# Optimization experiments

Hardware: AMD Instinct MI355X
Metric: run time of the kernel (lower is better)

The kernel has to match this reference:

```python
import jax, jax.numpy as jnp
import numpy as np

B_GRAPHS = 32   # number of graphs in the batch (static)
HEADS = 8
EPS = 1e-8


def _layer_norm(x, g, b):
    mu = x.mean(-1, keepdims=True)
    var = x.var(-1, keepdims=True)
    return (x - mu) * jax.lax.rsqrt(var + 1e-5) * g + b


def setup_inputs() -> dict:
    key = jax.random.key(0)
    ks = jax.random.split(key, 16)
    N, C, d, M = 5120, 128, 16, 256
    E = N * 16
    f32 = jnp.float32
    sc_c = 1.0 / np.sqrt(C)
    inp = {
        'x': jax.random.normal(ks[0], (N, C), f32),
        'pe_re': jax.random.normal(ks[1], (N, d), f32),
        'pe_im': jax.random.normal(ks[2], (N, d), f32),
        'wq': jax.random.normal(ks[3], (C, C), f32) * sc_c,
        'bq': jnp.zeros((C,), f32),
        'wk': jax.random.normal(ks[4], (C, C), f32) * sc_c,
        'bk': jnp.zeros((C,), f32),
        'wv': jax.random.normal(ks[5], (C, C), f32) * sc_c,
        'bv': jnp.zeros((C,), f32),
        'wo': jax.random.normal(ks[6], (C, C), f32) * sc_c,
        'bo': jnp.zeros((C,), f32),
        'pe_w1': jax.random.normal(ks[7], (4 * d, 2 * d), f32) * (1.0 / np.sqrt(4 * d)),
        'pe_b1': jnp.zeros((2 * d,), f32),
        'pe_w2': jax.random.normal(ks[8], (2 * d, HEADS), f32) * (1.0 / np.sqrt(2 * d)),
        'pe_b2': jnp.zeros((HEADS,), f32),
        'mlp_w1': jax.random.normal(ks[9], (C, 2 * C), f32) * sc_c,
        'mlp_b1': jnp.zeros((2 * C,), f32),
        'mlp_w2': jax.random.normal(ks[10], (2 * C, C), f32) * (1.0 / np.sqrt(2 * C)),
        'mlp_b2': jnp.zeros((C,), f32),
        'ln2_g': jnp.ones((C,), f32),
        'ln2_b': jnp.zeros((C,), f32),
        'ln3_g': jnp.ones((C,), f32),
        'ln3_b': jnp.zeros((C,), f32),
        'batch': jnp.sort(jax.random.randint(ks[11], (N,), 0, B_GRAPHS, jnp.int32)),
        'edge_index': jax.random.randint(ks[12], (2, E), 0, N, jnp.int32),
        'nmax': M,
    }
    return inp


def reference(x, pe_re, pe_im, wq, bq, wk, bk, wv, bv, wo, bo,
              pe_w1, pe_b1, pe_w2, pe_b2, mlp_w1, mlp_b1, mlp_w2, mlp_b2,
              ln2_g, ln2_b, ln3_g, ln3_b, batch, edge_index, nmax):
    N, C = x.shape
    H = HEADS
    dh = C // H
    M = nmax

    # --- to_dense_batch: ragged [N,*] -> dense [B, M, *] + mask ---
    counts = jax.ops.segment_sum(jnp.ones((N,), jnp.int32), batch, num_segments=B_GRAPHS)
    offsets = jnp.concatenate([jnp.zeros((1,), jnp.int32), jnp.cumsum(counts)[:-1]])
    intra = jnp.arange(N, dtype=jnp.int32) - offsets[batch]
    hd = jnp.zeros((B_GRAPHS, M, C), x.dtype).at[batch, intra].set(x)
    ar = jnp.zeros((B_GRAPHS, M, pe_re.shape[1]), x.dtype).at[batch, intra].set(pe_re)
    ai = jnp.zeros((B_GRAPHS, M, pe_im.shape[1]), x.dtype).at[batch, intra].set(pe_im)
    mask = jnp.zeros((B_GRAPHS, M), bool).at[batch, intra].set(True)

    # --- pairwise complex-angle PE bias ---
    pn = jnp.sqrt(ar * ar + ai * ai + EPS)                 # [B,M,d] complex_norm
    denom = pn[:, :, None, :] * pn[:, None, :, :] + EPS    # [B,M,M,d]
    # z_i * conj(z_j) normalized -> cos/sin of pairwise angle
    real = (ar[:, :, None, :] * ar[:, None, :, :] + ai[:, :, None, :] * ai[:, None, :, :]) / denom
    imag = (ai[:, :, None, :] * ar[:, None, :, :] - ar[:, :, None, :] * ai[:, None, :, :]) / denom
    pni = jnp.broadcast_to(pn[:, :, None, :], real.shape)
    pnj = jnp.broadcast_to(pn[:, None, :, :], real.shape)
    bias_in = jnp.concatenate([pni, pnj, real, imag], axis=-1)       # [B,M,M,4d]
    hb = jax.nn.relu(bias_in @ pe_w1 + pe_b1) @ pe_w2 + pe_b2        # [B,M,M,H]
    # torch: bias.transpose(1,-1) swaps dims 1 and 3 -> [B,H,M,M]
    bias = jnp.transpose(hb, (0, 3, 2, 1))                           # [B,H,q,k]

    # --- multi-head attention with float bias + key padding mask ---
    q = (hd @ wq + bq).reshape(B_GRAPHS, M, H, dh)
    k = (hd @ wk + bk).reshape(B_GRAPHS, M, H, dh)
    v = (hd @ wv + bv).reshape(B_GRAPHS, M, H, dh)
    scores = jnp.einsum('bihd,bjhd->bhij', q, k) / np.sqrt(dh) + bias
    scores = jnp.where(mask[:, None, None, :], scores, -1e9)
    attn = jax.nn.softmax(scores, axis=-1)
    o = jnp.einsum('bhij,bjhd->bihd', attn, v).reshape(B_GRAPHS, M, C)
    o = o @ wo + bo

    # --- back to ragged, residual, norms, FFN ---
    h = o[batch, intra] + x
    h = _layer_norm(h, ln2_g, ln2_b)
    out = h + (jax.nn.relu(h @ mlp_w1 + mlp_b1) @ mlp_w2 + mlp_b2)
    out = _layer_norm(out, ln3_g, ln3_b)
    return out
```

## Files before the change

### kernel.cpp

```cpp
#include <hip/hip_runtime.h>

#define N_NODES 5120
#define C_DIM   128
#define D_PE    16
#define M_MAX   256
#define B_G     32
#define H_HEADS 8
#define DH      16
#define EPS_PE  1e-8f
#define QT      2
#define SCP     264

#define WS_COUNTS   0
#define WS_OFFSETS  32
#define WS_INTRA    64
#define WS_MASK     5184
#define WS_CN       13376
#define WS_PN       275520
#define WS_KFHI     406592
#define WS_KFLO     668736
#define WS_QM       799808
#define WS_KM       1848384
#define WS_VM       2896960
#define WS_OATT     3945536
#define WS_HLN      4994112
#define WS_FFNH     5649472
#define WS_BIAS     6960192
#define WS_WPK_HI   15348800
#define WS_WPK_LO   15414336
#define WS_ZERO_FLOATS 13376

#define WOFF_O   49152
#define WOFF_W1  65536
#define WOFF_W2  98304

typedef __attribute__((ext_vector_type(8))) short bf8_t;
typedef __attribute__((ext_vector_type(4))) float f4_t;

__device__ inline short f2bf(float f) {
    union { float f; unsigned u; } v; v.f = f;
    unsigned r = (v.u + 0x7FFF + ((v.u >> 16) & 1)) >> 16;
    return (short)r;
}
__device__ inline float bf2f(short h) {
    union { unsigned u; float f; } v; v.u = ((unsigned)(unsigned short)h) << 16;
    return v.f;
}
__device__ inline unsigned pack2(short a, short b) {
    return (unsigned)(unsigned short)a | ((unsigned)(unsigned short)b << 16);
}
__device__ inline bf8_t bf8_from2(uint2 a, uint2 b) {
    bf8_t o;
    o[0]=(short)a.x; o[1]=(short)(a.x>>16); o[2]=(short)a.y; o[3]=(short)(a.y>>16);
    o[4]=(short)b.x; o[5]=(short)(b.x>>16); o[6]=(short)b.y; o[7]=(short)(b.y>>16);
    return o;
}

__global__ __launch_bounds__(256) void setup_kernel(
    const int* __restrict__ batch, int* __restrict__ counts_o,
    int* __restrict__ offsets, int* __restrict__ intra)
{
    __shared__ int cnt[B_G];
    __shared__ int off[B_G];
    const int t = threadIdx.x;
    if (t < B_G) cnt[t] = 0;
    __syncthreads();
    for (int n = t; n < N_NODES; n += 256) atomicAdd(&cnt[batch[n]], 1);
    __syncthreads();
    if (t == 0) { int s = 0; for (int b = 0; b < B_G; ++b) { off[b] = s; s += cnt[b]; } }
    __syncthreads();
    if (t < B_G) { offsets[t] = off[t]; counts_o[t] = cnt[t]; }
    for (int n = t; n < N_NODES; n += 256) intra[n] = n - off[batch[n]];
}

__global__ __launch_bounds__(256) void prep_kernel(
    const float* __restrict__ pre, const float* __restrict__ pim,
    const int* __restrict__ batch, const int* __restrict__ intra,
    float* __restrict__ pn, float* __restrict__ cn,
    unsigned short* __restrict__ kf_hi, unsigned short* __restrict__ kf_lo,
    int* __restrict__ mask)
{
    const int idx = blockIdx.x * 256 + threadIdx.x;
    const int n = idx >> 4, dd = idx & 15;
    const int b = batch[n], m = intra[n];
    const size_t cell = (size_t)b * M_MAX + m;
    const float a = pre[(size_t)n * D_PE + dd], bb = pim[(size_t)n * D_PE + dd];
    const float p = sqrtf(a * a + bb * bb + EPS_PE);
    const float inv = 1.f / p;
    const float cr = a * inv, ci = bb * inv;
    pn[cell * 16 + dd] = p;
    cn[cell * 32 + dd]      = cr;
    cn[cell * 32 + 16 + dd] = ci;
    const size_t hb = cell * 64, lb = cell * 32;
    short crh = f2bf(cr), cih = f2bf(ci);
    kf_hi[hb + dd]      = (unsigned short)crh;
    kf_hi[hb + 16 + dd] = (unsigned short)cih;
    kf_hi[hb + 32 + dd] = (unsigned short)f2bf(p);
    kf_hi[hb + 48 + dd] = (dd == 0) ? (unsigned short)f2bf(1.f) : 0;
    kf_lo[lb + dd]      = (unsigned short)f2bf(cr - bf2f(crh));
    kf_lo[lb + 16 + dd] = (unsigned short)f2bf(ci - bf2f(cih));
    if (dd == 0) mask[cell] = 1;
}

__global__ __launch_bounds__(256) void wpack_kernel(
    const float* __restrict__ wq, const float* __restrict__ wk,
    const float* __restrict__ wv, const float* __restrict__ wo,
    const float* __restrict__ w1, const float* __restrict__ w2,
    unsigned short* __restrict__ hi, unsigned short* __restrict__ lo)
{
    const int tid = blockIdx.x * 256 + threadIdx.x;
    const int tile = tid >> 6, lane = tid & 63;
    const float* W; int N, ltile; size_t off;
    if (tile < 128) {
        const int wi = tile >> 5; ltile = tile & 31; N = 128;
        W = (wi == 0) ? wq : (wi == 1) ? wk : (wi == 2) ? wv : wo;
        off = (size_t)wi * 16384;
    } else if (tile < 192) { ltile = tile - 128; N = 256; W = w1; off = WOFF_W1; }
    else                   { ltile = tile - 192; N = 128; W = w2; off = WOFF_W2; }
    const int NT = N / 16;
    const int kt = ltile / NT, nt = ltile % NT;
    const int col = nt * 16 + (lane & 15);
    const int k0  = kt * 32 + (lane >> 4) * 8;
    bf8_t vhi, vlo;
    #pragma unroll
    for (int e = 0; e < 8; ++e) {
        const float v = W[(size_t)(k0 + e) * N + col];
        const short h = f2bf(v);
        vhi[e] = h; vlo[e] = f2bf(v - bf2f(h));
    }
    const size_t toff = off + ((size_t)ltile * 64 + lane) * 8;
    *(bf8_t*)(hi + toff) = vhi;
    *(bf8_t*)(lo + toff) = vlo;
}

template<int K, int N>
__device__ inline void mgemm_core(
    const float* __restrict__ Arow,
    const unsigned short* __restrict__ hi, const unsigned short* __restrict__ lo,
    int lane, f4_t* acc)
{
    constexpr int NT = N / 16, KT = K / 32;
    const int g = lane >> 4;
    #pragma unroll
    for (int kt = 0; kt < KT; ++kt) {
        const float* ap = Arow + kt * 32 + g * 8;
        const float4 a0 = *(const float4*)ap;
        const float4 a1 = *(const float4*)(ap + 4);
        const float av[8] = {a0.x, a0.y, a0.z, a0.w, a1.x, a1.y, a1.z, a1.w};
        bf8_t ahi, alo;
        #pragma unroll
        for (int e = 0; e < 8; ++e) {
            const short h = f2bf(av[e]);
            ahi[e] = h; alo[e] = f2bf(av[e] - bf2f(h));
        }
        #pragma unroll
        for (int nt = 0; nt < NT; ++nt) {
            const size_t toff = ((size_t)(kt * NT + nt) * 64 + lane) * 8;
            const bf8_t bhi = *(const bf8_t*)(hi + toff);
            const bf8_t blo = *(const bf8_t*)(lo + toff);
            acc[nt] = __builtin_amdgcn_mfma_f32_16x16x32_bf16(ahi, bhi, acc[nt], 0, 0, 0);
            acc[nt] = __builtin_amdgcn_mfma_f32_16x16x32_bf16(alo, bhi, acc[nt], 0, 0, 0);
            acc[nt] = __builtin_amdgcn_mfma_f32_16x16x32_bf16(ahi, blo, acc[nt], 0, 0, 0);
        }
    }
}

__global__ __launch_bounds__(256) void qkv_node_kernel(
    const float* __restrict__ x,
    const unsigned short* __restrict__ hi, const unsigned short* __restrict__ lo,
    const float* __restrict__ bq, const float* __restrict__ bk, const float* __restrict__ bv,
    const int* __restrict__ batch, const int* __restrict__ intra,
    float* __restrict__ qm, float* __restrict__ km, float* __restrict__ vm)
{
    const int sel = blockIdx.y;
    const float* bias = (sel == 0) ? bq : (sel == 1) ? bk : bv;
    float* out = (sel == 0) ? qm : (sel == 1) ? km : vm;
    const unsigned short* whi = hi + (size_t)sel * 16384;
    const unsigned short* wlo = lo + (size_t)sel * 16384;

    const int rb = blockIdx.x * 64;
    const int w = threadIdx.x >> 6, lane = threadIdx.x & 63;
    const int lj = lane & 15, g = lane >> 4;
    const int arow = rb + w * 16 + lj;

    f4_t acc[8];
    #pragma unroll
    for (int nt = 0; nt < 8; ++nt) acc[nt] = (f4_t){0.f, 0.f, 0.f, 0.f};
    mgemm_core<128, 128>(x + (size_t)arow * 128, whi, wlo, lane, acc);

    const int orow0 = rb + w * 16 + g * 4;
    int dst[4];
    #pragma unroll
    for (int r = 0; r < 4; ++r) {
        const int nr = orow0 + r;
        dst[r] = batch[nr] * M_MAX + intra[nr];
    }
    #pragma unroll
    for (int nt = 0; nt < 8; ++nt) {
        const int col = nt * 16 + lj;
        const float bv_ = bias[col];
        #pragma unroll
        for (int r = 0; r < 4; ++r)
            out[(size_t)dst[r] * 128 + col] = acc[nt][r] + bv_;
    }
}

template<int K, int N, bool RELU>
__global__ __launch_bounds__(256) void mgemm_kernel(
    const float* __restrict__ A,
    const unsigned short* __restrict__ hi, const unsigned short* __restrict__ lo,
    const float* __restrict__ bias, float* __restrict__ out)
{
    constexpr int NT = N / 16;
    const int rb = blockIdx.x * 64;
    const int w = threadIdx.x >> 6, lane = threadIdx.x & 63;
    const int lj = lane & 15, g = lane >> 4;
    const int arow = rb + w * 16 + lj;

    f4_t acc[NT];
    #pragma unroll
    for (int nt = 0; nt < NT; ++nt) acc[nt] = (f4_t){0.f, 0.f, 0.f, 0.f};
    mgemm_core<K, N>(A + (size_t)arow * K, hi, lo, lane, acc);

    const int orow0 = rb + w * 16 + g * 4;
    #pragma unroll
    for (int nt = 0; nt < NT; ++nt) {
        const int col = nt * 16 + lj;
        const float bv = bias[col];
        #pragma unroll
        for (int r = 0; r < 4; ++r) {
            float v = acc[nt][r] + bv;
            if (RELU) v = fmaxf(v, 0.f);
            out[(size_t)(orow0 + r) * N + col] = v;
        }
    }
}

template<int K, bool GATHER_A>
__global__ __launch_bounds__(256) void gemm_res_ln_kernel(
    const float* __restrict__ A,
    const unsigned short* __restrict__ hi, const unsigned short* __restrict__ lo,
    const float* __restrict__ bias, const float* __restrict__ res,
    const int* __restrict__ batch, const int* __restrict__ intra,
    const float* __restrict__ lng, const float* __restrict__ lnb,
    float* __restrict__ out)
{
    __shared__ float sOut[64][133];
    __shared__ float red_s[64][4];
    __shared__ float red_q[64][4];

    const int rb = blockIdx.x * 64;
    const int w = threadIdx.x >> 6, lane = threadIdx.x & 63;
    const int lj = lane & 15, g = lane >> 4;
    const int arow = rb + w * 16 + lj;
    const size_t asrc = GATHER_A ? (size_t)(batch[arow] * M_MAX + intra[arow]) : (size_t)arow;

    f4_t acc[8];
    #pragma unroll
    for (int nt = 0; nt < 8; ++nt) acc[nt] = (f4_t){0.f, 0.f, 0.f, 0.f};
    mgemm_core<K, 128>(A + asrc * K, hi, lo, lane, acc);

    const int lrow0 = w * 16 + g * 4;
    #pragma unroll
    for (int nt = 0; nt < 8; ++nt) {
        const int col = nt * 16 + lj;
        const float bv = bias[col];
        #pragma unroll
        for (int r = 0; r < 4; ++r)
            sOut[lrow0 + r][col] = acc[nt][r] + bv;
    }
    __syncthreads();

    const int row = threadIdx.x >> 2, seg = threadIdx.x & 3;
    const int n = rb + row;
    float s = 0.f, sq = 0.f;
    #pragma unroll
    for (int i = 0; i < 32; ++i) {
        const int c = 4 * i + seg;
        const float v = sOut[row][c] + res[(size_t)n * 128 + c];
        sOut[row][c] = v;
        s += v; sq += v * v;
    }
    red_s[row][seg] = s; red_q[row][seg] = sq;
    __syncthreads();
    s  = red_s[row][0] + red_s[row][1] + red_s[row][2] + red_s[row][3];
    sq = red_q[row][0] + red_q[row][1] + red_q[row][2] + red_q[row][3];
    const float mu  = s * (1.f / 128.f);
    const float var = sq * (1.f / 128.f) - mu * mu;
    const float sc  = rsqrtf(var + 1e-5f);
    #pragma unroll
    for (int i = 0; i < 32; ++i) {
        const int c = 4 * i + seg;
        out[(size_t)n * 128 + c] = (sOut[row][c] - mu) * sc * lng[c] + lnb[c];
    }
}

__global__ __launch_bounds__(512) void bias_kernel(
    const float* __restrict__ cn, const float* __restrict__ pn,
    const unsigned short* __restrict__ kf_hi, const unsigned short* __restrict__ kf_lo,
    const float* __restrict__ w1, const float* __restrict__ b1,
    const float* __restrict__ w2, const float* __restrict__ b2,
    const int* __restrict__ counts,
    unsigned short* __restrict__ bias_out)
{
    const int b  = blockIdx.y;
    const int i0 = blockIdx.x * 16;
    if (i0 >= counts[b]) return;

    __shared__ float sW1T[32][65];
    __shared__ float s_cn[16][32];
    __shared__ float s_pn[16][16];
    __shared__ uint2 s_scr[8][16][10];

    const int t  = threadIdx.x;

    for (int idx = t; idx < 2048; idx += 512) {
        int f = idx >> 5, hh = idx & 31;
        sW1T[hh][f] = w1[f * 32 + hh];
    }
    { int il = t >> 5, c = t & 31;
      s_cn[il][c] = cn[((size_t)(b * 256 + i0 + il)) * 32 + c]; }
    if (t < 256) { int il = t >> 4, dd = t & 15;
      s_pn[il][dd] = pn[((size_t)(b * 256 + i0 + il)) * 16 + dd]; }
    __syncthreads();

    const int w    = t >> 6;
    const int lane = t & 63;
    const int lj   = lane & 15;
    const int g    = lane >> 4;

    bf8_t a2f;
    #pragma unroll
    for (int e = 0; e < 8; ++e) {
        float v = (lj < 8) ? w2[(g * 8 + e) * 8 + lj] : 0.f;
        a2f[e] = f2bf(v);
    }
    float b2v0 = 0.f, b2v1 = 0.f, b2v2 = 0.f, b2v3 = 0.f;
    if (g < 2) { b2v0 = b2[g*4+0]; b2v1 = b2[g*4+1]; b2v2 = b2[g*4+2]; b2v3 = b2[g*4+3]; }

    for (int ii = 0; ii < 2; ++ii) {
        const int il = w * 2 + ii;
        const int i  = i0 + il;

        float vrow0 = b1[lj], vrow1 = b1[16 + lj];
        #pragma unroll
        for (int dd = 0; dd < 16; ++dd) {
            float p = s_pn[il][dd];
            vrow0 = fmaf(sW1T[lj][16 + dd],      p, vrow0);
            vrow1 = fmaf(sW1T[16 + lj][16 + dd], p, vrow1);
        }

        bf8_t a0hi0, a0lo0, a1f0, a0hi1, a0lo1, a1f1;
        #pragma unroll
        for (int e = 0; e < 8; ++e) {
            const int dd = (g & 1) * 8 + e;
            const float cr = s_cn[il][dd], ci = s_cn[il][16 + dd];
            {
                float wr = sW1T[lj][32 + dd], wi = sW1T[lj][48 + dd];
                float val = (g < 2) ? (wr * cr - wi * ci) : (wr * ci + wi * cr);
                short hi = f2bf(val);
                a0hi0[e] = hi; a0lo0[e] = f2bf(val - bf2f(hi));
                float v1 = (g < 2) ? sW1T[lj][g * 8 + e]
                                   : ((g == 2 && e == 0) ? vrow0 : 0.f);
                a1f0[e] = f2bf(v1);
            }
            {
                float wr = sW1T[16 + lj][32 + dd], wi = sW1T[16 + lj][48 + dd];
                float val = (g < 2) ? (wr * cr - wi * ci) : (wr * ci + wi * cr);
                short hi = f2bf(val);
                a0hi1[e] = hi; a0lo1[e] = f2bf(val - bf2f(hi));
                float v1 = (g < 2) ? sW1T[16 + lj][g * 8 + e]
                                   : ((g == 2 && e == 0) ? vrow1 : 0.f);
                a1f1[e] = f2bf(v1);
            }
        }

        for (int jt = 0; jt < 16; ++jt) {
            const size_t node = (size_t)b * 256 + jt * 16 + lj;
            const bf8_t* ph = (const bf8_t*)(kf_hi + node * 64);
            const bf8_t* pl = (const bf8_t*)(kf_lo + node * 32);
            bf8_t b0hi = ph[g];
            bf8_t b0lo = pl[g];
            bf8_t b1f  = ph[4 + g];

            f4_t acc0 = {0.f, 0.f, 0.f, 0.f}, acc1 = {0.f, 0.f, 0.f, 0.f};
            acc0 = __builtin_amdgcn_mfma_f32_16x16x32_bf16(a0hi0, b0hi, acc0, 0, 0, 0);
            acc0 = __builtin_amdgcn_mfma_f32_16x16x32_bf16(a0hi0, b0lo, acc0, 0, 0, 0);
            acc0 = __builtin_amdgcn_mfma_f32_16x16x32_bf16(a0lo0, b0hi, acc0, 0, 0, 0);
            acc0 = __builtin_amdgcn_mfma_f32_16x16x32_bf16(a1f0,  b1f,  acc0, 0, 0, 0);
            acc1 = __builtin_amdgcn_mfma_f32_16x16x32_bf16(a0hi1, b0hi, acc1, 0, 0, 0);
            acc1 = __builtin_amdgcn_mfma_f32_16x16x32_bf16(a0hi1, b0lo, acc1, 0, 0, 0);
            acc1 = __builtin_amdgcn_mfma_f32_16x16x32_bf16(a0lo1, b0hi, acc1, 0, 0, 0);
            acc1 = __builtin_amdgcn_mfma_f32_16x16x32_bf16(a1f1,  b1f,  acc1, 0, 0, 0);

            uint2 w0, w1p;
            w0.x  = pack2(f2bf(fmaxf(acc0[0], 0.f)), f2bf(fmaxf(acc0[1], 0.f)));
            w0.y  = pack2(f2bf(fmaxf(acc0[2], 0.f)), f2bf(fmaxf(acc0[3], 0.f)));
            w1p.x = pack2(f2bf(fmaxf(acc1[0], 0.f)), f2bf(fmaxf(acc1[1], 0.f)));
            w1p.y = pack2(f2bf(fmaxf(acc1[2], 0.f)), f2bf(fmaxf(acc1[3], 0.f)));
            s_scr[w][lj][g]     = w0;
            s_scr[w][lj][4 + g] = w1p;
            __builtin_amdgcn_s_waitcnt(0);

            uint2 q0 = s_scr[w][lj][2 * g];
            uint2 q1 = s_scr[w][lj][2 * g + 1];
            bf8_t hb = bf8_from2(q0, q1);

            f4_t acc2 = {0.f, 0.f, 0.f, 0.f};
            acc2 = __builtin_amdgcn_mfma_f32_16x16x32_bf16(a2f, hb, acc2, 0, 0, 0);

            if (g < 2) {
                uint2 st;
                st.x = pack2(f2bf(acc2[0] + b2v0), f2bf(acc2[1] + b2v1));
                st.y = pack2(f2bf(acc2[2] + b2v2), f2bf(acc2[3] + b2v3));
                size_t idx = (((size_t)b * 256 + i) * 256 + jt * 16 + lj) * 8 + g * 4;
                *(uint2*)(bias_out + idx) = st;
            }
        }
    }
}

__global__ __launch_bounds__(256) void attn_kernel(
    const float* __restrict__ qm, const float* __restrict__ km, const float* __restrict__ vm,
    const int* __restrict__ mask, const unsigned short* __restrict__ bias,
    const int* __restrict__ counts,
    float* __restrict__ o_att)
{
    const int b  = blockIdx.y;
    const int i0 = blockIdx.x * QT;
    if (i0 >= counts[b]) return;
    const int t  = threadIdx.x;
    const int j  = t;

    __shared__ float s_q[QT][C_DIM];
    __shared__ float s_sc[QT][H_HEADS][SCP];

    {
        const int qi = t >> 7, c = t & 127;
        s_q[qi][c] = qm[((size_t)(b * 256 + i0 + qi)) * C_DIM + c];
    }
    __syncthreads();

    const int mj = mask[b * M_MAX + j];
    uint4 bu[QT];
    #pragma unroll
    for (int qi = 0; qi < QT; ++qi)
        bu[qi] = *(const uint4*)(bias + (((size_t)(b * 256 + i0 + qi)) * 256 + j) * 8);

    const float* krow = km + ((size_t)(b * 256 + j)) * C_DIM;
    #pragma unroll
    for (int h = 0; h < 8; ++h) {
        float kv[DH];
        #pragma unroll
        for (int q4 = 0; q4 < 4; ++q4) {
            float4 v = ((const float4*)(krow + h * DH))[q4];
            kv[q4*4+0]=v.x; kv[q4*4+1]=v.y; kv[q4*4+2]=v.z; kv[q4*4+3]=v.w;
        }
        #pragma unroll
        for (int qi = 0; qi < QT; ++qi) {
            float dot = 0.f;
            #pragma unroll
            for (int dd = 0; dd < DH; ++dd)
                dot = fmaf(s_q[qi][h * DH + dd], kv[dd], dot);
            const unsigned u = ((const unsigned*)&bu[qi])[h >> 1];
            const float bv = bf2f((short)((h & 1) ? (u >> 16) : (u & 0xffff)));
            s_sc[qi][h][j] = mj ? fmaf(dot, 0.25f, bv) : -1e9f;
        }
    }
    __syncthreads();

    {
        const int wave = t >> 6, lane = t & 63;
        for (int r = wave; r < QT * H_HEADS; r += 4) {
            float* row = ((float*)s_sc) + r * SCP;
            float x0 = row[lane], x1 = row[lane + 64], x2 = row[lane + 128], x3 = row[lane + 192];
            float mx = fmaxf(fmaxf(x0, x1), fmaxf(x2, x3));
            #pragma unroll
            for (int off = 32; off > 0; off >>= 1) mx = fmaxf(mx, __shfl_xor(mx, off, 64));
            float e0 = expf(x0 - mx), e1 = expf(x1 - mx), e2 = expf(x2 - mx), e3 = expf(x3 - mx);
            float s = e0 + e1 + e2 + e3;
            #pragma unroll
            for (int off = 32; off > 0; off >>= 1) s += __shfl_xor(s, off, 64);
            const float inv = 1.f / s;
            row[lane] = e0 * inv; row[lane + 64] = e1 * inv;
            row[lane + 128] = e2 * inv; row[lane + 192] = e3 * inv;
        }
    }
    __syncthreads();

    {
        const int c = t & 127;
        const int gq = t >> 7;
        const int h = c >> 4;
        const float* vb = vm + (size_t)b * M_MAX * C_DIM + c;
        float a0 = 0.f;
        for (int jj = 0; jj < M_MAX; jj += 4) {
            float4 pA = *(const float4*)&s_sc[gq][h][jj];
            a0 = fmaf(pA.x, vb[(size_t)(jj + 0) * C_DIM], a0);
            a0 = fmaf(pA.y, vb[(size_t)(jj + 1) * C_DIM], a0);
            a0 = fmaf(pA.z, vb[(size_t)(jj + 2) * C_DIM], a0);
            a0 = fmaf(pA.w, vb[(size_t)(jj + 3) * C_DIM], a0);
        }
        o_att[((size_t)(b * 256 + i0 + gq)) * C_DIM + c] = a0;
    }
}

extern "C" void kernel_launch(void* const* d_in, const int* in_sizes, int n_in,
                              void* d_out, int out_size, void* d_ws, size_t ws_size,
                              hipStream_t stream)
{
    const float* x      = (const float*)d_in[0];
    const float* pe_re  = (const float*)d_in[1];
    const float* pe_im  = (const float*)d_in[2];
    const float* wq     = (const float*)d_in[3];
    const float* bq     = (const float*)d_in[4];
    const float* wk     = (const float*)d_in[5];
    const float* bk     = (const float*)d_in[6];
    const float* wv     = (const float*)d_in[7];
    const float* bv     = (const float*)d_in[8];
    const float* wo     = (const float*)d_in[9];
    const float* bo     = (const float*)d_in[10];
    const float* pe_w1  = (const float*)d_in[11];
    const float* pe_b1  = (const float*)d_in[12];
    const float* pe_w2  = (const float*)d_in[13];
    const float* pe_b2  = (const float*)d_in[14];
    const float* mlp_w1 = (const float*)d_in[15];
    const float* mlp_b1 = (const float*)d_in[16];
    const float* mlp_w2 = (const float*)d_in[17];
    const float* mlp_b2 = (const float*)d_in[18];
    const float* ln2_g  = (const float*)d_in[19];
    const float* ln2_b  = (const float*)d_in[20];
    const float* ln3_g  = (const float*)d_in[21];
    const float* ln3_b  = (const float*)d_in[22];
    const int*   batch  = (const int*)d_in[23];

    float* ws = (float*)d_ws;
    int*   counts  = (int*)(ws + WS_COUNTS);
    int*   offsets = (int*)(ws + WS_OFFSETS);
    int*   intra   = (int*)(ws + WS_INTRA);
    int*   mask    = (int*)(ws + WS_MASK);
    float* cn   = ws + WS_CN;
    float* pn   = ws + WS_PN;
    unsigned short* kf_hi = (unsigned short*)(ws + WS_KFHI);
    unsigned short* kf_lo = (unsigned short*)(ws + WS_KFLO);
    float* qm   = ws + WS_QM;
    float* km   = ws + WS_KM;
    float* vm   = ws + WS_VM;
    float* oatt = ws + WS_OATT;
    float* hln  = ws + WS_HLN;
    float* ffnh = ws + WS_FFNH;
    unsigned short* bias = (unsigned short*)(ws + WS_BIAS);
    unsigned short* wpk_hi = (unsigned short*)(ws + WS_WPK_HI);
    unsigned short* wpk_lo = (unsigned short*)(ws + WS_WPK_LO);
    float* outp = (float*)d_out;

    hipMemsetAsync(d_ws, 0, (size_t)WS_ZERO_FLOATS * sizeof(float), stream);

    setup_kernel<<<1, 256, 0, stream>>>(batch, counts, offsets, intra);
    wpack_kernel<<<64, 256, 0, stream>>>(wq, wk, wv, wo, mlp_w1, mlp_w2, wpk_hi, wpk_lo);
    prep_kernel<<<320, 256, 0, stream>>>(pe_re, pe_im, batch, intra, pn, cn, kf_hi, kf_lo, mask);

    qkv_node_kernel<<<dim3(80, 3), 256, 0, stream>>>(x, wpk_hi, wpk_lo, bq, bk, bv,
                                                     batch, intra, qm, km, vm);

    bias_kernel<<<dim3(16, 32), 512, 0, stream>>>(cn, pn, kf_hi, kf_lo,
                                                  pe_w1, pe_b1, pe_w2, pe_b2, counts, bias);

    attn_kernel<<<dim3(M_MAX / QT, B_G), 256, 0, stream>>>(qm, km, vm, mask, bias, counts, oatt);

    gemm_res_ln_kernel<128, true><<<80, 256, 0, stream>>>(
        oatt, wpk_hi + WOFF_O, wpk_lo + WOFF_O, bo, x, batch, intra, ln2_g, ln2_b, hln);

    mgemm_kernel<128, 256, true><<<80, 256, 0, stream>>>(
        hln, wpk_hi + WOFF_W1, wpk_lo + WOFF_W1, mlp_b1, ffnh);

    gemm_res_ln_kernel<256, false><<<80, 256, 0, stream>>>(
        ffnh, wpk_hi + WOFF_W2, wpk_lo + WOFF_W2, mlp_b2, hln, batch, intra, ln3_g, ln3_b, outp);
}
```

Before: 325.1 us.

## Skip padded key columns in bias and attention, tile four queries per block

The bias kernel now loops only over key tiles that cover real nodes of the graph instead of all 16 tiles. The attention kernel processes four query rows per block instead of two, so each V element loaded is reused for two query rows per thread. Its PV loop is also cut short at the graph's real node count, rounded up to 4. Masked keys get zero softmax weight, so skipping them should be exact as long as the padded bias entries are not read anywhere else. Shared memory per attention block roughly doubles, which may lower occupancy.

```diff
diff --git a/kernel.cpp b/kernel.cpp
--- a/kernel.cpp
+++ b/kernel.cpp
@@ -8,7 +8,7 @@
 #define H_HEADS 8
 #define DH      16
 #define EPS_PE  1e-8f
-#define QT      2
+#define QT      4
 #define SCP     264
 
 #define WS_COUNTS   0
@@ -305,7 +305,9 @@
 {
     const int b  = blockIdx.y;
     const int i0 = blockIdx.x * 16;
-    if (i0 >= counts[b]) return;
+    const int cntb = counts[b];
+    if (i0 >= cntb) return;
+    const int jtN = (cntb + 15) >> 4;
 
     __shared__ float sW1T[32][65];
     __shared__ float s_cn[16][32];
@@ -375,7 +377,7 @@
             }
         }
 
-        for (int jt = 0; jt < 16; ++jt) {
+        for (int jt = 0; jt < jtN; ++jt) {
             const size_t node = (size_t)b * 256 + jt * 16 + lj;
             const bf8_t* ph = (const bf8_t*)(kf_hi + node * 64);
             const bf8_t* pl = (const bf8_t*)(kf_lo + node * 32);
@@ -428,15 +430,16 @@
 {
     const int b  = blockIdx.y;
     const int i0 = blockIdx.x * QT;
-    if (i0 >= counts[b]) return;
+    const int cntb = counts[b];
+    if (i0 >= cntb) return;
     const int t  = threadIdx.x;
     const int j  = t;
 
     __shared__ float s_q[QT][C_DIM];
     __shared__ float s_sc[QT][H_HEADS][SCP];
 
-    {
-        const int qi = t >> 7, c = t & 127;
+    for (int idx = t; idx < QT * C_DIM; idx += 256) {
+        const int qi = idx >> 7, c = idx & 127;
         s_q[qi][c] = qm[((size_t)(b * 256 + i0 + qi)) * C_DIM + c];
     }
     __syncthreads();
@@ -492,16 +495,24 @@
         const int c = t & 127;
         const int gq = t >> 7;
         const int h = c >> 4;
+        const int qA = gq * 2, qB = gq * 2 + 1;
+        const int jlim = (cntb + 3) & ~3;
         const float* vb = vm + (size_t)b * M_MAX * C_DIM + c;
-        float a0 = 0.f;
-        for (int jj = 0; jj < M_MAX; jj += 4) {
-            float4 pA = *(const float4*)&s_sc[gq][h][jj];
-            a0 = fmaf(pA.x, vb[(size_t)(jj + 0) * C_DIM], a0);
-            a0 = fmaf(pA.y, vb[(size_t)(jj + 1) * C_DIM], a0);
-            a0 = fmaf(pA.z, vb[(size_t)(jj + 2) * C_DIM], a0);
-            a0 = fmaf(pA.w, vb[(size_t)(jj + 3) * C_DIM], a0);
-        }
-        o_att[((size_t)(b * 256 + i0 + gq)) * C_DIM + c] = a0;
+        float a0 = 0.f, a1 = 0.f;
+        for (int jj = 0; jj < jlim; jj += 4) {
+            float4 pA = *(const float4*)&s_sc[qA][h][jj];
+            float4 pB = *(const float4*)&s_sc[qB][h][jj];
+            float v0 = vb[(size_t)(jj + 0) * C_DIM];
+            float v1 = vb[(size_t)(jj + 1) * C_DIM];
+            float v2 = vb[(size_t)(jj + 2) * C_DIM];
+            float v3 = vb[(size_t)(jj + 3) * C_DIM];
+            a0 = fmaf(pA.x, v0, a0); a0 = fmaf(pA.y, v1, a0);
+            a0 = fmaf(pA.z, v2, a0); a0 = fmaf(pA.w, v3, a0);
+            a1 = fmaf(pB.x, v0, a1); a1 = fmaf(pB.y, v1, a1);
+            a1 = fmaf(pB.z, v2, a1); a1 = fmaf(pB.w, v3, a1);
+        }
+        o_att[((size_t)(b * 256 + i0 + qA)) * C_DIM + c] = a0;
+        o_att[((size_t)(b * 256 + i0 + qB)) * C_DIM + c] = a1;
     }
 }
 
```

New measurement: 296.1 us. -8.9%, faster.
